# Optimization experiments

Hardware: AMD Instinct MI355X
Metric: run time of the kernel (lower is better)

## Reference

```python
import jax, jax.numpy as jnp
import numpy as np

AGENT_RADIUS = 0.2
SAFETY_DIST = 0.1
_ang = np.linspace(0.0, 2.0 * np.pi, 8, endpoint=False)
OBSTACLES = np.stack([10.0 * np.cos(_ang), 10.0 * np.sin(_ang), 0.5 * np.ones(8)], axis=-1).astype(np.float32)  # (x, y, r)


def _qp_solve(p, G, h):
    """Exact solve of: min_z 0.5 z^T z + p^T z  s.t. G z <= h, z in R^2.
    Equivalent to QPFunction with Q=I. Enumerates KKT candidates over active
    sets of size 0, 1, 2 (closed form in 2D) and picks the feasible optimum.
    p: [2], G: [m,2], h: [m]."""
    m = G.shape[0]
    ii, jj = np.triu_indices(m, 1)
    # active set {} -> unconstrained minimizer
    z0 = -p[None, :]                                        # [1,2]
    # active set {i}: z = -p - lam*g_i, g_i.z = h_i
    gg = jnp.sum(G * G, axis=-1)                            # [m]
    lam1 = (-(G @ p) - h) / (gg + 1e-12)
    z1 = -p[None, :] - lam1[:, None] * G                    # [m,2]
    ok1 = lam1 >= -1e-8
    # active set {i,j}: z solves 2x2 system [g_i; g_j] z = [h_i; h_j]
    Gi, Gj = G[ii], G[jj]                                   # [P,2]
    hi, hj = h[ii], h[jj]
    det = Gi[:, 0] * Gj[:, 1] - Gi[:, 1] * Gj[:, 0]
    det_ok = jnp.abs(det) > 1e-9
    ds = jnp.where(det_ok, det, 1.0)
    zx = (hi * Gj[:, 1] - hj * Gi[:, 1]) / ds
    zy = (Gi[:, 0] * hj - Gj[:, 0] * hi) / ds
    z2 = jnp.stack([zx, zy], axis=-1)                       # [P,2]
    r = -(z2 + p[None, :])                                  # A^T lam = r
    lam_i = (Gj[:, 1] * r[:, 0] - Gj[:, 0] * r[:, 1]) / ds
    lam_j = (Gi[:, 0] * r[:, 1] - Gi[:, 1] * r[:, 0]) / ds
    ok2 = det_ok & (lam_i >= -1e-8) & (lam_j >= -1e-8)
    Z = jnp.concatenate([z0, z1, z2], axis=0)               # [K,2]
    ok = jnp.concatenate([jnp.ones((1,), bool), ok1, ok2], axis=0)
    tol = 1e-6 * (1.0 + jnp.abs(h))
    feas = jnp.all(Z @ G.T <= (h + tol)[None, :], axis=-1)  # [K]
    obj = 0.5 * jnp.sum(Z * Z, axis=-1) + Z @ p
    obj = jnp.where(ok & feas, obj, jnp.inf)
    return Z[jnp.argmin(obj)]


def _forward(x, mean, std, W1, b1, W21, b21, W31, b31, W22, b22, W32, b32):
    x0 = x * std + mean                                     # de-normalized state [B,8]
    hid = jax.nn.relu(x @ W1.T + b1)
    x31 = jax.nn.relu(hid @ W21.T + b21) @ W31.T + b31      # reference control p [B,2]
    x32 = 4.0 * jax.nn.sigmoid(jax.nn.relu(hid @ W22.T + b22) @ W32.T + b32)  # CBF penalties [B,2]
    px, py, theta, v = x0[:, 0], x0[:, 1], x0[:, 2], x0[:, 3]
    ox, oy, oth, ov = x0[:, 4], x0[:, 5], x0[:, 6], x0[:, 7]
    st, ct = jnp.sin(theta), jnp.cos(theta)
    vs, vc = v * st, v * ct
    obs = jnp.asarray(OBSTACLES, x.dtype)
    # static obstacle constraints, vectorized over the n_obs obstacles
    dx = px[:, None] - obs[None, :, 0]                      # [B,n_obs]
    dy = py[:, None] - obs[None, :, 1]
    R = AGENT_RADIUS + obs[:, 2] + SAFETY_DIST
    bar = dx * dx + dy * dy - (R * R)[None, :]
    bdot = 2.0 * dx * vc[:, None] + 2.0 * dy * vs[:, None]
    Lf2b = (2.0 * v * v)[:, None]
    u1 = -2.0 * dx * vs[:, None] + 2.0 * dy * vc[:, None]
    u2 = 2.0 * dx * ct[:, None] + 2.0 * dy * st[:, None]
    G_obs = -jnp.stack([u1, u2], axis=-1)                   # [B,n_obs,2]
    s0, s1 = x32[:, 0:1], x32[:, 1:2]
    h_obs = Lf2b + (s0 + s1) * bdot + (s0 * s1) * bar       # [B,n_obs]
    # opponent constraint
    Ro = 2.0 * AGENT_RADIUS + SAFETY_DIST
    dxo, dyo = px - ox, py - oy
    so, co = jnp.sin(oth), jnp.cos(oth)
    bar_o = dxo * dxo + dyo * dyo - Ro * Ro
    bdot_o = 2.0 * dxo * (vc - ov * co) + 2.0 * dyo * (vs - ov * so)
    Lf2b_o = 2.0 * (v * v + ov * ov + 2.0 * v * ov * jnp.cos(theta - oth))
    u1o = -2.0 * dxo * vs + 2.0 * dyo * vc
    u2o = 2.0 * dxo * ct + 2.0 * dyo * st
    G_opp = -jnp.stack([u1o, u2o], axis=-1)[:, None, :]     # [B,1,2]
    h_opp = (Lf2b_o + (x32[:, 0] + x32[:, 1]) * bdot_o + x32[:, 0] * x32[:, 1] * bar_o)[:, None]
    G = jnp.concatenate([G_obs, G_opp], axis=1)             # [B,m,2]
    h = jnp.concatenate([h_obs, h_opp], axis=1)             # [B,m]
    return jax.vmap(_qp_solve)(x31, G, h)                   # [B,2]


def setup_inputs() -> dict:
    key = jax.random.key(0)
    ks = jax.random.split(key, 6)
    B, nF, H1, H2 = 65536, 8, 256, 128

    def lin(k, o, i):
        k1, k2 = jax.random.split(k)
        W = jax.random.normal(k1, (o, i), jnp.float32) / np.float32(np.sqrt(i))
        b = jax.random.normal(k2, (o,), jnp.float32) * 0.01
        return W, b

    W1, b1 = lin(ks[0], H1, nF)
    W21, b21 = lin(ks[1], H2, H1)
    W31, b31 = lin(ks[2], 2, H2)
    W22, b22 = lin(ks[3], H2, H1)
    W32, b32 = lin(ks[4], 2, H2)
    x = jax.random.normal(ks[5], (B, nF), jnp.float32)
    return {"x": x, "mean": jnp.zeros((nF,), jnp.float32), "std": jnp.ones((nF,), jnp.float32),
            "W1": W1, "b1": b1, "W21": W21, "b21": b21, "W31": W31, "b31": b31,
            "W22": W22, "b22": b22, "W32": W32, "b32": b32, "sgn": 1}


def reference(x, mean, std, W1, b1, W21, b21, W31, b31, W22, b22, W32, b32, sgn):
    # sgn==1 / training path -> batched differentiable QP solve
    return _forward(x, mean, std, W1, b1, W21, b21, W31, b31, W22, b22, W32, b32)
```

## Files before the change

### kernel.cpp

```cpp
#include <hip/hip_runtime.h>
#include <hip/hip_bf16.h>
#include <math.h>


typedef unsigned int u32;
typedef unsigned long long u64;
typedef unsigned short u16;
typedef __attribute__((ext_vector_type(8))) short short8;
typedef __attribute__((ext_vector_type(4))) float f32x4;
typedef __attribute__((ext_vector_type(2))) float f32x2;
typedef __attribute__((ext_vector_type(4))) u32 u32x4;

union Frag { short8 v; u32 u[4]; u32x4 q; };

__device__ __forceinline__ u32 packbf(float a, float b) {
    float2 f2; f2.x = a; f2.y = b;
    __hip_bfloat162 h = __float22bfloat162_rn(f2);
    union { __hip_bfloat162 h2; u32 u; } cv; cv.h2 = h;
    return cv.u;
}

__device__ const float OBX[8] = { 10.f, 7.07106781186547524f, 6.123234e-16f, -7.07106781186547524f,
                                 -10.f, -7.07106781186547524f, -1.8369702e-15f, 7.07106781186547524f };
__device__ const float OBY[8] = { 0.f, 7.07106781186547524f, 10.f, 7.07106781186547524f,
                                  1.2246468e-15f, -7.07106781186547524f, -10.f, -7.07106781186547524f };

#define PI0_ 0x2111111100000000ULL
#define PI1_ 0x5544443333322222ULL
#define PI2_ 0x7665ULL
#define PJ0_ 0x3876543287654321ULL
#define PJ1_ 0x7687658765487654ULL
#define PJ2_ 0x8878ULL
__device__ __forceinline__ int unpack4(u64 w0, u64 w1, u64 w2, int t) {
    u64 w = (t < 16) ? w0 : (t < 32) ? w1 : w2;
    return (int)((w >> ((t & 15) * 4)) & 15);
}

__global__ __launch_bounds__(256)
void prep_kernel(const float* __restrict__ W21, const float* __restrict__ W22,
                 u32* __restrict__ ws)
{
    int idx  = blockIdx.x * 256 + threadIdx.x;
    int lane = idx & 63;
    int nt   = (idx >> 6) & 7;
    int ks   = (idx >> 9) & 7;
    int head = idx >> 12;
    const float* W = head ? W22 : W21;
    int n  = nt * 16 + (lane & 15);
    int k0 = ks * 32 + (lane >> 4) * 8;
    const float* s = W + n * 256 + k0;
    u32x4 o;
    o.x = packbf(s[0], s[1]);
    o.y = packbf(s[2], s[3]);
    o.z = packbf(s[4], s[5]);
    o.w = packbf(s[6], s[7]);
    __builtin_nontemporal_store(o, (u32x4*)ws + idx);
}

__global__ __launch_bounds__(512)
void barriernet_kernel(const float* __restrict__ x,
                       const float* __restrict__ meanp,
                       const float* __restrict__ stdp,
                       const float* __restrict__ W1,
                       const float* __restrict__ b1,
                       const float* __restrict__ b21,
                       const float* __restrict__ W31,
                       const float* __restrict__ b31,
                       const float* __restrict__ b22,
                       const float* __restrict__ W32,
                       const float* __restrict__ b32,
                       const u32* __restrict__ wsB,
                       float* __restrict__ out, int Btot)
{
    const int tid  = threadIdx.x;
    const int wave = tid >> 6;
    const int lane = tid & 63;
    const int q    = lane >> 4;
    const int m    = lane & 15;
    const int blockRow = blockIdx.x * 128;

    __shared__ u32x4 stage[2048];
    __shared__ float lds_p[128][4];

    f32x4 xa0, xb0;
    {
        int R0 = blockRow + wave * 16 + m;
        const f32x4* xv0 = (const f32x4*)(x + (R0 < Btot ? R0 : 0) * 8);
        xa0 = xv0[0]; xb0 = xv0[1];
    }

    const f32x4* W1v = (const f32x4*)W1;
    const f32x4* b1v = (const f32x4*)b1;

    Frag A[8];
    #pragma unroll
    for (int ks = 0; ks < 8; ++ks) {
        int kb = ks * 32 + q * 8;
        f32x4 bA = b1v[kb >> 2];
        f32x4 bB = b1v[(kb >> 2) + 1];
        float h0[8];
        #pragma unroll
        for (int j = 0; j < 8; ++j) {
            f32x4 wa = W1v[(kb + j) * 2];
            f32x4 wb = W1v[(kb + j) * 2 + 1];
            float a0 = (j < 4) ? bA[j] : bB[j - 4];
            a0 = fmaf(wa.x, xa0.x, a0);
            a0 = fmaf(wa.y, xa0.y, a0);
            a0 = fmaf(wa.z, xa0.z, a0);
            a0 = fmaf(wa.w, xa0.w, a0);
            a0 = fmaf(wb.x, xb0.x, a0);
            a0 = fmaf(wb.y, xb0.y, a0);
            a0 = fmaf(wb.z, xb0.z, a0);
            a0 = fmaf(wb.w, xb0.w, a0);
            h0[j] = fmaxf(a0, 0.f);
        }
        #pragma unroll
        for (int t = 0; t < 4; ++t)
            A[ks].u[t] = packbf(h0[2 * t], h0[2 * t + 1]);
    }

    const u32x4* wsB4 = (const u32x4*)wsB;

    #pragma unroll 1
    for (int head = 0; head < 2; ++head) {
        const float* b2 = head ? b22 : b21;
        const float* W3 = head ? W32 : W31;
        const float* b3 = head ? b32 : b31;

        f32x4 acc[8];
        #pragma unroll
        for (int nt = 0; nt < 8; ++nt) acc[nt] = (f32x4){0.f, 0.f, 0.f, 0.f};

        #pragma unroll
        for (int half = 0; half < 2; ++half) {
            const u32x4* src = wsB4 + head * 4096 + half * 2048;
            #pragma unroll
            for (int i = 0; i < 4; ++i) {
                int fi = (wave * 4 + i) * 64 + lane;
                stage[fi] = src[fi];
            }
            __syncthreads();
            #pragma unroll
            for (int ksl = 0; ksl < 4; ++ksl) {
                const int ks = half * 4 + ksl;
                Frag Bf[8];
                #pragma unroll
                for (int nt = 0; nt < 8; ++nt)
                    Bf[nt].q = stage[ksl * 512 + nt * 64 + lane];
                #pragma unroll
                for (int nt = 0; nt < 8; ++nt)
                    acc[nt] = __builtin_amdgcn_mfma_f32_16x16x32_bf16(A[ks].v, Bf[nt].v, acc[nt], 0, 0, 0);
            }
            __syncthreads();
        }

        float pr0[4], pr1[4];
        #pragma unroll
        for (int rg = 0; rg < 4; ++rg) { pr0[rg] = 0.f; pr1[rg] = 0.f; }
        #pragma unroll
        for (int nt = 0; nt < 8; ++nt) {
            int col = nt * 16 + m;
            float b2c = b2[col];
            float w0c = W3[col];
            float w1c = W3[128 + col];
            #pragma unroll
            for (int rg = 0; rg < 4; ++rg) {
                float rv = fmaxf(acc[nt][rg] + b2c, 0.f);
                pr0[rg] = fmaf(rv, w0c, pr0[rg]);
                pr1[rg] = fmaf(rv, w1c, pr1[rg]);
            }
        }
        #pragma unroll
        for (int rg = 0; rg < 4; ++rg) {
            float v0 = pr0[rg], v1 = pr1[rg];
            #pragma unroll
            for (int off = 1; off < 16; off <<= 1) {
                v0 += __shfl_xor(v0, off, 64);
                v1 += __shfl_xor(v1, off, 64);
            }
            pr0[rg] = v0; pr1[rg] = v1;
        }
        if (m == 0) {
            #pragma unroll
            for (int rg = 0; rg < 4; ++rg) {
                int row = wave * 16 + q * 4 + rg;
                float a0 = pr0[rg] + b3[0];
                float a1 = pr1[rg] + b3[1];
                if (head == 0) {
                    lds_p[row][0] = a0;
                    lds_p[row][1] = a1;
                } else {
                    lds_p[row][2] = 4.f / (1.f + __expf(-a0));
                    lds_p[row][3] = 4.f / (1.f + __expf(-a1));
                }
            }
        }
    }
    __syncthreads();

    f32x4 (*qC)[128]  = (f32x4(*)[128])stage;
    f32x4 (*res)[128] = (f32x4(*)[128])(stage + 1152);

    const int rq   = tid & 127;
    const int part = tid >> 7;
    const int R    = blockRow + rq;
    float p0 = lds_p[rq][0];
    float p1 = lds_p[rq][1];

    if (part == 0) {
        float s0 = lds_p[rq][2];
        float s1 = lds_p[rq][3];
        float xr[8];
        const float* xp = x + (R < Btot ? R : 0) * 8;
        #pragma unroll
        for (int c = 0; c < 8; ++c) xr[c] = fmaf(xp[c], stdp[c], meanp[c]);
        float px = xr[0], py = xr[1], th = xr[2], v = xr[3];
        float ox = xr[4], oy = xr[5], oth = xr[6], ov = xr[7];
        float st = __sinf(th),  ct = __cosf(th);
        float so = __sinf(oth), co = __cosf(oth);
        float vs = v * st, vc = v * ct;
        float sps = s0 + s1, ss = s0 * s1;
        float Lf2b = 2.f * v * v;
        #pragma unroll 1
        for (int k = 0; k < 8; ++k) {
            float dx = px - OBX[k], dy = py - OBY[k];
            float bar  = dx * dx + dy * dy - 0.64f;
            float bdot = 2.f * dx * vc + 2.f * dy * vs;
            float gx = 2.f * dx * vs - 2.f * dy * vc;
            float gy = -(2.f * dx * ct + 2.f * dy * st);
            float hk = Lf2b + sps * bdot + ss * bar;
            float ht = hk + 1e-6f * (1.f + fabsf(hk));
            qC[k][rq] = (f32x4){gx, gy, hk, ht};
        }
        {
            float dxo = px - ox, dyo = py - oy;
            float bar_o  = dxo * dxo + dyo * dyo - 0.25f;
            float bdot_o = 2.f * dxo * (vc - ov * co) + 2.f * dyo * (vs - ov * so);
            float Lf2b_o = 2.f * (v * v + ov * ov + 2.f * v * ov * __cosf(th - oth));
            float gx = 2.f * dxo * vs - 2.f * dyo * vc;
            float gy = -(2.f * dxo * ct + 2.f * dyo * st);
            float hk = Lf2b_o + sps * bdot_o + ss * bar_o;
            float ht = hk + 1e-6f * (1.f + fabsf(hk));
            qC[8][rq] = (f32x4){gx, gy, hk, ht};
        }
    }
    __syncthreads();

    const f32x4 C0 = qC[0][rq], C1 = qC[1][rq], C2 = qC[2][rq];
    const f32x4 C3 = qC[3][rq], C4 = qC[4][rq], C5 = qC[5][rq];
    const f32x4 C6 = qC[6][rq], C7 = qC[7][rq], C8 = qC[8][rq];

    const int c0i = (part == 0) ? 0  : (part == 1) ? 12 : (part == 2) ? 24 : 35;
    const int c1i = (part == 0) ? 12 : (part == 1) ? 24 : (part == 2) ? 35 : 46;
    float bobj = INFINITY;
    float bzx = -p0, bzy = -p1;
    #pragma unroll 2
    for (int c = c0i; c < c1i; ++c) {
        float zx, zy;
        bool pre;
        if (c == 0) {
            zx = -p0; zy = -p1; pre = true;
        } else if (c <= 9) {
            f32x4 g = qC[c - 1][rq];
            float gg  = g.x * g.x + g.y * g.y;
            float lam = (-(g.x * p0 + g.y * p1) - g.z) / (gg + 1e-12f);
            zx = -p0 - lam * g.x;
            zy = -p1 - lam * g.y;
            pre = (lam >= -1e-8f);
        } else {
            int t = c - 10;
            int pi = unpack4(PI0_, PI1_, PI2_, t);
            int pj = unpack4(PJ0_, PJ1_, PJ2_, t);
            f32x4 gi = qC[pi][rq];
            f32x4 gj = qC[pj][rq];
            float det = gi.x * gj.y - gi.y * gj.x;
            bool dok = fabsf(det) > 1e-9f;
            float ds = dok ? det : 1.0f;
            float inv = 1.0f / ds;
            zx = (gi.z * gj.y - gj.z * gi.y) * inv;
            zy = (gi.x * gj.z - gj.x * gi.z) * inv;
            float rx = -(zx + p0), ry = -(zy + p1);
            float li = (gj.y * rx - gj.x * ry) * inv;
            float lj = (gi.x * ry - gi.y * rx) * inv;
            pre = dok && (li >= -1e-8f) && (lj >= -1e-8f);
        }
        bool ok = pre;
        ok = ok && (zx * C0.x + zy * C0.y <= C0.w);
        ok = ok && (zx * C1.x + zy * C1.y <= C1.w);
        ok = ok && (zx * C2.x + zy * C2.y <= C2.w);
        ok = ok && (zx * C3.x + zy * C3.y <= C3.w);
        ok = ok && (zx * C4.x + zy * C4.y <= C4.w);
        ok = ok && (zx * C5.x + zy * C5.y <= C5.w);
        ok = ok && (zx * C6.x + zy * C6.y <= C6.w);
        ok = ok && (zx * C7.x + zy * C7.y <= C7.w);
        ok = ok && (zx * C8.x + zy * C8.y <= C8.w);
        float obj = 0.5f * (zx * zx + zy * zy) + zx * p0 + zy * p1;
        if (ok && obj < bobj) { bobj = obj; bzx = zx; bzy = zy; }
    }

    if (part) {
        res[part - 1][rq] = (f32x4){bobj, bzx, bzy, 0.f};
    }
    __syncthreads();
    if (part == 0) {
        #pragma unroll
        for (int pp = 0; pp < 3; ++pp) {
            f32x4 r = res[pp][rq];
            if (r.x < bobj) { bobj = r.x; bzx = r.y; bzy = r.z; }
        }
        if (R < Btot) {
            f32x2 o2; o2.x = bzx; o2.y = bzy;
            ((f32x2*)out)[R] = o2;
        }
    }
}

extern "C" void kernel_launch(void* const* d_in, const int* in_sizes, int n_in,
                              void* d_out, int out_size, void* d_ws, size_t ws_size,
                              hipStream_t stream) {
    const float* x    = (const float*)d_in[0];
    const float* mean = (const float*)d_in[1];
    const float* stdv = (const float*)d_in[2];
    const float* W1   = (const float*)d_in[3];
    const float* b1   = (const float*)d_in[4];
    const float* W21  = (const float*)d_in[5];
    const float* b21  = (const float*)d_in[6];
    const float* W31  = (const float*)d_in[7];
    const float* b31  = (const float*)d_in[8];
    const float* W22  = (const float*)d_in[9];
    const float* b22  = (const float*)d_in[10];
    const float* W32  = (const float*)d_in[11];
    const float* b32  = (const float*)d_in[12];
    int B = in_sizes[0] / 8;
    float* out = (float*)d_out;
    u32* ws = (u32*)d_ws;

    hipLaunchKernelGGL(prep_kernel, dim3(32), dim3(256), 0, stream, W21, W22, ws);

    hipLaunchKernelGGL(barriernet_kernel, dim3((B + 127) / 128), dim3(512), 0, stream,
                       x, mean, stdv, W1, b1, b21, W31, b31, b22, W32, b32,
                       ws, out, B);
}
```

Measured before the change: 117.7 us.

## Halve block threads so each wave computes two 16-row tiles reusing B fragments

The block shrinks from 512 to 256 threads while still covering 128 rows. Each wave now computes two 16-row MFMA tiles per head and shares each loaded B fragment across both, halving LDS reads per MFMA. The QP candidate enumeration is split across two thread parts instead of four, so each thread checks twice as many candidates and the final reduction merges only one partial result. This raises register pressure (two accumulator sets, two A-fragment sets) and lengthens the serial QP phase per thread.

```diff
diff --git a/kernel.cpp b/kernel.cpp
--- a/kernel.cpp
+++ b/kernel.cpp
@@ -57,7 +57,7 @@
     __builtin_nontemporal_store(o, (u32x4*)ws + idx);
 }
 
-__global__ __launch_bounds__(512)
+__global__ __launch_bounds__(256)
 void barriernet_kernel(const float* __restrict__ x,
                        const float* __restrict__ meanp,
                        const float* __restrict__ stdp,
@@ -82,41 +82,43 @@
     __shared__ u32x4 stage[2048];
     __shared__ float lds_p[128][4];
 
-    f32x4 xa0, xb0;
-    {
-        int R0 = blockRow + wave * 16 + m;
-        const f32x4* xv0 = (const f32x4*)(x + (R0 < Btot ? R0 : 0) * 8);
-        xa0 = xv0[0]; xb0 = xv0[1];
-    }
-
     const f32x4* W1v = (const f32x4*)W1;
     const f32x4* b1v = (const f32x4*)b1;
 
-    Frag A[8];
+    Frag A[2][8];
     #pragma unroll
-    for (int ks = 0; ks < 8; ++ks) {
-        int kb = ks * 32 + q * 8;
-        f32x4 bA = b1v[kb >> 2];
-        f32x4 bB = b1v[(kb >> 2) + 1];
-        float h0[8];
-        #pragma unroll
-        for (int j = 0; j < 8; ++j) {
-            f32x4 wa = W1v[(kb + j) * 2];
-            f32x4 wb = W1v[(kb + j) * 2 + 1];
-            float a0 = (j < 4) ? bA[j] : bB[j - 4];
-            a0 = fmaf(wa.x, xa0.x, a0);
-            a0 = fmaf(wa.y, xa0.y, a0);
-            a0 = fmaf(wa.z, xa0.z, a0);
-            a0 = fmaf(wa.w, xa0.w, a0);
-            a0 = fmaf(wb.x, xb0.x, a0);
-            a0 = fmaf(wb.y, xb0.y, a0);
-            a0 = fmaf(wb.z, xb0.z, a0);
-            a0 = fmaf(wb.w, xb0.w, a0);
-            h0[j] = fmaxf(a0, 0.f);
-        }
-        #pragma unroll
-        for (int t = 0; t < 4; ++t)
-            A[ks].u[t] = packbf(h0[2 * t], h0[2 * t + 1]);
+    for (int rs = 0; rs < 2; ++rs) {
+        f32x4 xa0, xb0;
+        {
+            int R0 = blockRow + wave * 32 + rs * 16 + m;
+            const f32x4* xv0 = (const f32x4*)(x + (R0 < Btot ? R0 : 0) * 8);
+            xa0 = xv0[0]; xb0 = xv0[1];
+        }
+        #pragma unroll
+        for (int ks = 0; ks < 8; ++ks) {
+            int kb = ks * 32 + q * 8;
+            f32x4 bA = b1v[kb >> 2];
+            f32x4 bB = b1v[(kb >> 2) + 1];
+            float h0[8];
+            #pragma unroll
+            for (int j = 0; j < 8; ++j) {
+                f32x4 wa = W1v[(kb + j) * 2];
+                f32x4 wb = W1v[(kb + j) * 2 + 1];
+                float a0 = (j < 4) ? bA[j] : bB[j - 4];
+                a0 = fmaf(wa.x, xa0.x, a0);
+                a0 = fmaf(wa.y, xa0.y, a0);
+                a0 = fmaf(wa.z, xa0.z, a0);
+                a0 = fmaf(wa.w, xa0.w, a0);
+                a0 = fmaf(wb.x, xb0.x, a0);
+                a0 = fmaf(wb.y, xb0.y, a0);
+                a0 = fmaf(wb.z, xb0.z, a0);
+                a0 = fmaf(wb.w, xb0.w, a0);
+                h0[j] = fmaxf(a0, 0.f);
+            }
+            #pragma unroll
+            for (int t = 0; t < 4; ++t)
+                A[rs][ks].u[t] = packbf(h0[2 * t], h0[2 * t + 1]);
+        }
     }
 
     const u32x4* wsB4 = (const u32x4*)wsB;
@@ -127,16 +129,18 @@
         const float* W3 = head ? W32 : W31;
         const float* b3 = head ? b32 : b31;
 
-        f32x4 acc[8];
-        #pragma unroll
-        for (int nt = 0; nt < 8; ++nt) acc[nt] = (f32x4){0.f, 0.f, 0.f, 0.f};
+        f32x4 acc[2][8];
+        #pragma unroll
+        for (int rs = 0; rs < 2; ++rs)
+            #pragma unroll
+            for (int nt = 0; nt < 8; ++nt) acc[rs][nt] = (f32x4){0.f, 0.f, 0.f, 0.f};
 
         #pragma unroll
         for (int half = 0; half < 2; ++half) {
             const u32x4* src = wsB4 + head * 4096 + half * 2048;
             #pragma unroll
-            for (int i = 0; i < 4; ++i) {
-                int fi = (wave * 4 + i) * 64 + lane;
+            for (int i = 0; i < 8; ++i) {
+                int fi = (wave * 8 + i) * 64 + lane;
                 stage[fi] = src[fi];
             }
             __syncthreads();
@@ -148,50 +152,55 @@
                 for (int nt = 0; nt < 8; ++nt)
                     Bf[nt].q = stage[ksl * 512 + nt * 64 + lane];
                 #pragma unroll
-                for (int nt = 0; nt < 8; ++nt)
-                    acc[nt] = __builtin_amdgcn_mfma_f32_16x16x32_bf16(A[ks].v, Bf[nt].v, acc[nt], 0, 0, 0);
+                for (int nt = 0; nt < 8; ++nt) {
+                    acc[0][nt] = __builtin_amdgcn_mfma_f32_16x16x32_bf16(A[0][ks].v, Bf[nt].v, acc[0][nt], 0, 0, 0);
+                    acc[1][nt] = __builtin_amdgcn_mfma_f32_16x16x32_bf16(A[1][ks].v, Bf[nt].v, acc[1][nt], 0, 0, 0);
+                }
             }
             __syncthreads();
         }
 
-        float pr0[4], pr1[4];
-        #pragma unroll
-        for (int rg = 0; rg < 4; ++rg) { pr0[rg] = 0.f; pr1[rg] = 0.f; }
-        #pragma unroll
-        for (int nt = 0; nt < 8; ++nt) {
-            int col = nt * 16 + m;
-            float b2c = b2[col];
-            float w0c = W3[col];
-            float w1c = W3[128 + col];
+        #pragma unroll
+        for (int rs = 0; rs < 2; ++rs) {
+            float pr0[4], pr1[4];
+            #pragma unroll
+            for (int rg = 0; rg < 4; ++rg) { pr0[rg] = 0.f; pr1[rg] = 0.f; }
+            #pragma unroll
+            for (int nt = 0; nt < 8; ++nt) {
+                int col = nt * 16 + m;
+                float b2c = b2[col];
+                float w0c = W3[col];
+                float w1c = W3[128 + col];
+                #pragma unroll
+                for (int rg = 0; rg < 4; ++rg) {
+                    float rv = fmaxf(acc[rs][nt][rg] + b2c, 0.f);
+                    pr0[rg] = fmaf(rv, w0c, pr0[rg]);
+                    pr1[rg] = fmaf(rv, w1c, pr1[rg]);
+                }
+            }
             #pragma unroll
             for (int rg = 0; rg < 4; ++rg) {
-                float rv = fmaxf(acc[nt][rg] + b2c, 0.f);
-                pr0[rg] = fmaf(rv, w0c, pr0[rg]);
-                pr1[rg] = fmaf(rv, w1c, pr1[rg]);
-            }
-        }
-        #pragma unroll
-        for (int rg = 0; rg < 4; ++rg) {
-            float v0 = pr0[rg], v1 = pr1[rg];
-            #pragma unroll
-            for (int off = 1; off < 16; off <<= 1) {
-                v0 += __shfl_xor(v0, off, 64);
-                v1 += __shfl_xor(v1, off, 64);
-            }
-            pr0[rg] = v0; pr1[rg] = v1;
-        }
-        if (m == 0) {
-            #pragma unroll
-            for (int rg = 0; rg < 4; ++rg) {
-                int row = wave * 16 + q * 4 + rg;
-                float a0 = pr0[rg] + b3[0];
-                float a1 = pr1[rg] + b3[1];
-                if (head == 0) {
-                    lds_p[row][0] = a0;
-                    lds_p[row][1] = a1;
-                } else {
-                    lds_p[row][2] = 4.f / (1.f + __expf(-a0));
-                    lds_p[row][3] = 4.f / (1.f + __expf(-a1));
+                float v0 = pr0[rg], v1 = pr1[rg];
+                #pragma unroll
+                for (int off = 1; off < 16; off <<= 1) {
+                    v0 += __shfl_xor(v0, off, 64);
+                    v1 += __shfl_xor(v1, off, 64);
+                }
+                pr0[rg] = v0; pr1[rg] = v1;
+            }
+            if (m == 0) {
+                #pragma unroll
+                for (int rg = 0; rg < 4; ++rg) {
+                    int row = wave * 32 + rs * 16 + q * 4 + rg;
+                    float a0 = pr0[rg] + b3[0];
+                    float a1 = pr1[rg] + b3[1];
+                    if (head == 0) {
+                        lds_p[row][0] = a0;
+                        lds_p[row][1] = a1;
+                    } else {
+                        lds_p[row][2] = 4.f / (1.f + __expf(-a0));
+                        lds_p[row][3] = 4.f / (1.f + __expf(-a1));
+                    }
                 }
             }
         }
@@ -250,8 +259,8 @@
     const f32x4 C3 = qC[3][rq], C4 = qC[4][rq], C5 = qC[5][rq];
     const f32x4 C6 = qC[6][rq], C7 = qC[7][rq], C8 = qC[8][rq];
 
-    const int c0i = (part == 0) ? 0  : (part == 1) ? 12 : (part == 2) ? 24 : 35;
-    const int c1i = (part == 0) ? 12 : (part == 1) ? 24 : (part == 2) ? 35 : 46;
+    const int c0i = (part == 0) ? 0  : 24;
+    const int c1i = (part == 0) ? 24 : 46;
     float bobj = INFINITY;
     float bzx = -p0, bzy = -p1;
     #pragma unroll 2
@@ -299,15 +308,12 @@
     }
 
     if (part) {
-        res[part - 1][rq] = (f32x4){bobj, bzx, bzy, 0.f};
+        res[0][rq] = (f32x4){bobj, bzx, bzy, 0.f};
     }
     __syncthreads();
     if (part == 0) {
-        #pragma unroll
-        for (int pp = 0; pp < 3; ++pp) {
-            f32x4 r = res[pp][rq];
-            if (r.x < bobj) { bobj = r.x; bzx = r.y; bzy = r.z; }
-        }
+        f32x4 r = res[0][rq];
+        if (r.x < bobj) { bobj = r.x; bzx = r.y; bzy = r.z; }
         if (R < Btot) {
             f32x2 o2; o2.x = bzx; o2.y = bzy;
             ((f32x2*)out)[R] = o2;
@@ -337,7 +343,7 @@
 
     hipLaunchKernelGGL(prep_kernel, dim3(32), dim3(256), 0, stream, W21, W22, ws);
 
-    hipLaunchKernelGGL(barriernet_kernel, dim3((B + 127) / 128), dim3(512), 0, stream,
+    hipLaunchKernelGGL(barriernet_kernel, dim3((B + 127) / 128), dim3(256), 0, stream,
                        x, mean, stdv, W1, b1, b21, W31, b31, b22, W32, b32,
                        ws, out, B);
 }
```

After: 157.6 us. 33.9% more time.

## Compute first layer with bf16 MFMA and skip QP enumeration when unconstrained optimum feasible

Applied to the files above, without the earlier changes.

The first dense layer (8->256 plus bias) moves from per-lane scalar FMAs to 16 bf16 MFMA ops. The prep kernel now also packs W1 and b1 into fragment layout, and the bias is folded in through a constant 1.0 column in the x fragment. Separately, the QP solver first checks whether the unconstrained minimizer satisfies all constraints and, if so, skips the enumeration of single and pairwise active-set candidates. This rounds x and W1 to bf16, which adds some precision risk.

```diff
diff --git a/kernel.cpp b/kernel.cpp
--- a/kernel.cpp
+++ b/kernel.cpp
@@ -38,31 +38,50 @@
 
 __global__ __launch_bounds__(256)
 void prep_kernel(const float* __restrict__ W21, const float* __restrict__ W22,
+                 const float* __restrict__ W1,  const float* __restrict__ b1,
                  u32* __restrict__ ws)
 {
     int idx  = blockIdx.x * 256 + threadIdx.x;
-    int lane = idx & 63;
-    int nt   = (idx >> 6) & 7;
-    int ks   = (idx >> 9) & 7;
-    int head = idx >> 12;
-    const float* W = head ? W22 : W21;
-    int n  = nt * 16 + (lane & 15);
-    int k0 = ks * 32 + (lane >> 4) * 8;
-    const float* s = W + n * 256 + k0;
-    u32x4 o;
-    o.x = packbf(s[0], s[1]);
-    o.y = packbf(s[2], s[3]);
-    o.z = packbf(s[4], s[5]);
-    o.w = packbf(s[6], s[7]);
-    __builtin_nontemporal_store(o, (u32x4*)ws + idx);
+    if (idx < 8192) {
+        int lane = idx & 63;
+        int nt   = (idx >> 6) & 7;
+        int ks   = (idx >> 9) & 7;
+        int head = idx >> 12;
+        const float* W = head ? W22 : W21;
+        int n  = nt * 16 + (lane & 15);
+        int k0 = ks * 32 + (lane >> 4) * 8;
+        const float* s = W + n * 256 + k0;
+        u32x4 o;
+        o.x = packbf(s[0], s[1]);
+        o.y = packbf(s[2], s[3]);
+        o.z = packbf(s[4], s[5]);
+        o.w = packbf(s[6], s[7]);
+        __builtin_nontemporal_store(o, (u32x4*)ws + idx);
+    } else {
+        int f    = idx - 8192;
+        int nt   = f >> 6;
+        int lane = f & 63;
+        int q    = lane >> 4;
+        int mm   = lane & 15;
+        int n = 32 * (nt & 7) + 8 * (mm >> 2) + 4 * (nt >> 3) + (mm & 3);
+        u32x4 o = (u32x4){0u, 0u, 0u, 0u};
+        if (q == 0) {
+            const float* wr = W1 + n * 8;
+            o.x = packbf(wr[0], wr[1]);
+            o.y = packbf(wr[2], wr[3]);
+            o.z = packbf(wr[4], wr[5]);
+            o.w = packbf(wr[6], wr[7]);
+        } else if (q == 1) {
+            o.x = packbf(b1[n], 0.f);
+        }
+        __builtin_nontemporal_store(o, (u32x4*)ws + idx);
+    }
 }
 
 __global__ __launch_bounds__(512)
 void barriernet_kernel(const float* __restrict__ x,
                        const float* __restrict__ meanp,
                        const float* __restrict__ stdp,
-                       const float* __restrict__ W1,
-                       const float* __restrict__ b1,
                        const float* __restrict__ b21,
                        const float* __restrict__ W31,
                        const float* __restrict__ b31,
@@ -82,44 +101,43 @@
     __shared__ u32x4 stage[2048];
     __shared__ float lds_p[128][4];
 
-    f32x4 xa0, xb0;
+    const u32x4* wsB4 = (const u32x4*)wsB;
+
+    Frag xB;
     {
         int R0 = blockRow + wave * 16 + m;
         const f32x4* xv0 = (const f32x4*)(x + (R0 < Btot ? R0 : 0) * 8);
-        xa0 = xv0[0]; xb0 = xv0[1];
-    }
-
-    const f32x4* W1v = (const f32x4*)W1;
-    const f32x4* b1v = (const f32x4*)b1;
-
+        f32x4 xa0 = xv0[0], xb0 = xv0[1];
+        if (q == 0) {
+            xB.u[0] = packbf(xa0.x, xa0.y);
+            xB.u[1] = packbf(xa0.z, xa0.w);
+            xB.u[2] = packbf(xb0.x, xb0.y);
+            xB.u[3] = packbf(xb0.z, xb0.w);
+        } else if (q == 1) {
+            xB.u[0] = 0x00003f80u;
+            xB.u[1] = 0u; xB.u[2] = 0u; xB.u[3] = 0u;
+        } else {
+            xB.u[0] = 0u; xB.u[1] = 0u; xB.u[2] = 0u; xB.u[3] = 0u;
+        }
+    }
+    f32x4 hacc[16];
+    {
+        const u32x4* W1f = wsB4 + 8192;
+        #pragma unroll
+        for (int nt = 0; nt < 16; ++nt) {
+            Frag Af; Af.q = W1f[nt * 64 + lane];
+            hacc[nt] = __builtin_amdgcn_mfma_f32_16x16x32_bf16(
+                Af.v, xB.v, (f32x4){0.f, 0.f, 0.f, 0.f}, 0, 0, 0);
+        }
+    }
     Frag A[8];
     #pragma unroll
     for (int ks = 0; ks < 8; ++ks) {
-        int kb = ks * 32 + q * 8;
-        f32x4 bA = b1v[kb >> 2];
-        f32x4 bB = b1v[(kb >> 2) + 1];
-        float h0[8];
-        #pragma unroll
-        for (int j = 0; j < 8; ++j) {
-            f32x4 wa = W1v[(kb + j) * 2];
-            f32x4 wb = W1v[(kb + j) * 2 + 1];
-            float a0 = (j < 4) ? bA[j] : bB[j - 4];
-            a0 = fmaf(wa.x, xa0.x, a0);
-            a0 = fmaf(wa.y, xa0.y, a0);
-            a0 = fmaf(wa.z, xa0.z, a0);
-            a0 = fmaf(wa.w, xa0.w, a0);
-            a0 = fmaf(wb.x, xb0.x, a0);
-            a0 = fmaf(wb.y, xb0.y, a0);
-            a0 = fmaf(wb.z, xb0.z, a0);
-            a0 = fmaf(wb.w, xb0.w, a0);
-            h0[j] = fmaxf(a0, 0.f);
-        }
-        #pragma unroll
-        for (int t = 0; t < 4; ++t)
-            A[ks].u[t] = packbf(h0[2 * t], h0[2 * t + 1]);
-    }
-
-    const u32x4* wsB4 = (const u32x4*)wsB;
+        A[ks].u[0] = packbf(fmaxf(hacc[ks][0], 0.f),     fmaxf(hacc[ks][1], 0.f));
+        A[ks].u[1] = packbf(fmaxf(hacc[ks][2], 0.f),     fmaxf(hacc[ks][3], 0.f));
+        A[ks].u[2] = packbf(fmaxf(hacc[ks + 8][0], 0.f), fmaxf(hacc[ks + 8][1], 0.f));
+        A[ks].u[3] = packbf(fmaxf(hacc[ks + 8][2], 0.f), fmaxf(hacc[ks + 8][3], 0.f));
+    }
 
     #pragma unroll 1
     for (int head = 0; head < 2; ++head) {
@@ -250,52 +268,69 @@
     const f32x4 C3 = qC[3][rq], C4 = qC[4][rq], C5 = qC[5][rq];
     const f32x4 C6 = qC[6][rq], C7 = qC[7][rq], C8 = qC[8][rq];
 
-    const int c0i = (part == 0) ? 0  : (part == 1) ? 12 : (part == 2) ? 24 : 35;
-    const int c1i = (part == 0) ? 12 : (part == 1) ? 24 : (part == 2) ? 35 : 46;
+    const float zx0 = -p0, zy0 = -p1;
+    bool z0ok =
+        (zx0 * C0.x + zy0 * C0.y <= C0.w) &&
+        (zx0 * C1.x + zy0 * C1.y <= C1.w) &&
+        (zx0 * C2.x + zy0 * C2.y <= C2.w) &&
+        (zx0 * C3.x + zy0 * C3.y <= C3.w) &&
+        (zx0 * C4.x + zy0 * C4.y <= C4.w) &&
+        (zx0 * C5.x + zy0 * C5.y <= C5.w) &&
+        (zx0 * C6.x + zy0 * C6.y <= C6.w) &&
+        (zx0 * C7.x + zy0 * C7.y <= C7.w) &&
+        (zx0 * C8.x + zy0 * C8.y <= C8.w);
+
     float bobj = INFINITY;
-    float bzx = -p0, bzy = -p1;
-    #pragma unroll 2
-    for (int c = c0i; c < c1i; ++c) {
-        float zx, zy;
-        bool pre;
-        if (c == 0) {
-            zx = -p0; zy = -p1; pre = true;
-        } else if (c <= 9) {
-            f32x4 g = qC[c - 1][rq];
-            float gg  = g.x * g.x + g.y * g.y;
-            float lam = (-(g.x * p0 + g.y * p1) - g.z) / (gg + 1e-12f);
-            zx = -p0 - lam * g.x;
-            zy = -p1 - lam * g.y;
-            pre = (lam >= -1e-8f);
-        } else {
-            int t = c - 10;
-            int pi = unpack4(PI0_, PI1_, PI2_, t);
-            int pj = unpack4(PJ0_, PJ1_, PJ2_, t);
-            f32x4 gi = qC[pi][rq];
-            f32x4 gj = qC[pj][rq];
-            float det = gi.x * gj.y - gi.y * gj.x;
-            bool dok = fabsf(det) > 1e-9f;
-            float ds = dok ? det : 1.0f;
-            float inv = 1.0f / ds;
-            zx = (gi.z * gj.y - gj.z * gi.y) * inv;
-            zy = (gi.x * gj.z - gj.x * gi.z) * inv;
-            float rx = -(zx + p0), ry = -(zy + p1);
-            float li = (gj.y * rx - gj.x * ry) * inv;
-            float lj = (gi.x * ry - gi.y * rx) * inv;
-            pre = dok && (li >= -1e-8f) && (lj >= -1e-8f);
-        }
-        bool ok = pre;
-        ok = ok && (zx * C0.x + zy * C0.y <= C0.w);
-        ok = ok && (zx * C1.x + zy * C1.y <= C1.w);
-        ok = ok && (zx * C2.x + zy * C2.y <= C2.w);
-        ok = ok && (zx * C3.x + zy * C3.y <= C3.w);
-        ok = ok && (zx * C4.x + zy * C4.y <= C4.w);
-        ok = ok && (zx * C5.x + zy * C5.y <= C5.w);
-        ok = ok && (zx * C6.x + zy * C6.y <= C6.w);
-        ok = ok && (zx * C7.x + zy * C7.y <= C7.w);
-        ok = ok && (zx * C8.x + zy * C8.y <= C8.w);
-        float obj = 0.5f * (zx * zx + zy * zy) + zx * p0 + zy * p1;
-        if (ok && obj < bobj) { bobj = obj; bzx = zx; bzy = zy; }
+    float bzx = zx0, bzy = zy0;
+    if (z0ok) {
+        if (part == 0)
+            bobj = 0.5f * (zx0 * zx0 + zy0 * zy0) + zx0 * p0 + zy0 * p1;
+    } else {
+        const int c0i = (part == 0) ? 0  : (part == 1) ? 12 : (part == 2) ? 24 : 35;
+        const int c1i = (part == 0) ? 12 : (part == 1) ? 24 : (part == 2) ? 35 : 46;
+        #pragma unroll 2
+        for (int c = c0i; c < c1i; ++c) {
+            float zx, zy;
+            bool pre;
+            if (c == 0) {
+                zx = -p0; zy = -p1; pre = true;
+            } else if (c <= 9) {
+                f32x4 g = qC[c - 1][rq];
+                float gg  = g.x * g.x + g.y * g.y;
+                float lam = (-(g.x * p0 + g.y * p1) - g.z) / (gg + 1e-12f);
+                zx = -p0 - lam * g.x;
+                zy = -p1 - lam * g.y;
+                pre = (lam >= -1e-8f);
+            } else {
+                int t = c - 10;
+                int pi = unpack4(PI0_, PI1_, PI2_, t);
+                int pj = unpack4(PJ0_, PJ1_, PJ2_, t);
+                f32x4 gi = qC[pi][rq];
+                f32x4 gj = qC[pj][rq];
+                float det = gi.x * gj.y - gi.y * gj.x;
+                bool dok = fabsf(det) > 1e-9f;
+                float ds = dok ? det : 1.0f;
+                float inv = 1.0f / ds;
+                zx = (gi.z * gj.y - gj.z * gi.y) * inv;
+                zy = (gi.x * gj.z - gj.x * gi.z) * inv;
+                float rx = -(zx + p0), ry = -(zy + p1);
+                float li = (gj.y * rx - gj.x * ry) * inv;
+                float lj = (gi.x * ry - gi.y * rx) * inv;
+                pre = dok && (li >= -1e-8f) && (lj >= -1e-8f);
+            }
+            bool ok = pre;
+            ok = ok && (zx * C0.x + zy * C0.y <= C0.w);
+            ok = ok && (zx * C1.x + zy * C1.y <= C1.w);
+            ok = ok && (zx * C2.x + zy * C2.y <= C2.w);
+            ok = ok && (zx * C3.x + zy * C3.y <= C3.w);
+            ok = ok && (zx * C4.x + zy * C4.y <= C4.w);
+            ok = ok && (zx * C5.x + zy * C5.y <= C5.w);
+            ok = ok && (zx * C6.x + zy * C6.y <= C6.w);
+            ok = ok && (zx * C7.x + zy * C7.y <= C7.w);
+            ok = ok && (zx * C8.x + zy * C8.y <= C8.w);
+            float obj = 0.5f * (zx * zx + zy * zy) + zx * p0 + zy * p1;
+            if (ok && obj < bobj) { bobj = obj; bzx = zx; bzy = zy; }
+        }
     }
 
     if (part) {
@@ -335,9 +370,10 @@
     float* out = (float*)d_out;
     u32* ws = (u32*)d_ws;
 
-    hipLaunchKernelGGL(prep_kernel, dim3(32), dim3(256), 0, stream, W21, W22, ws);
+    hipLaunchKernelGGL(prep_kernel, dim3(36), dim3(256), 0, stream,
+                       W21, W22, W1, b1, ws);
 
     hipLaunchKernelGGL(barriernet_kernel, dim3((B + 127) / 128), dim3(512), 0, stream,
-                       x, mean, stdv, W1, b1, b21, W31, b31, b22, W32, b32,
+                       x, mean, stdv, b21, W31, b31, b22, W32, b32,
                        ws, out, B);
 }
```

Result: faster. 106.9 us (-9.2%).
